# Performance work log

Hardware: AMD Instinct MI355X
Metric: run time of the kernel (lower is better)

## Reference

```python
import jax, jax.numpy as jnp
import numpy as np

B, T, D = 2, 2048, 2048
H, KVH = 16, 4
HD = D // H            # 128
HALF = HD // 2         # 64
EPS = 1e-6


def zc_rmsnorm(x, scale):
    # zero-centred RMSNorm: (1+scale) * x / rms(x), rms in fp32
    rms = jnp.sqrt(jnp.mean(x.astype(jnp.float32) ** 2, axis=-1, keepdims=True) + EPS)
    return ((1.0 + scale) * x / rms).astype(x.dtype)


def apply_rope(x, cos, sin):
    # x: [B, h, T, HD]; cos/sin: [T, HALF]
    t = x.shape[2]
    c = cos[:t][None, None, :, :]
    s = sin[:t][None, None, :, :]
    x1, x2 = x[..., :HALF], x[..., HALF:]
    return jnp.concatenate([x1 * c - x2 * s, x2 * c + x1 * s], axis=-1)


def setup_inputs() -> dict:
    key = jax.random.key(0)
    ks = jax.random.split(key, 8)
    std = 0.02
    res_std = 0.02 / np.sqrt(2 * 24)
    q_input = jax.random.normal(ks[0], (B, T, D), jnp.float32)
    kv_input = jax.random.normal(ks[1], (B, T, D), jnp.float32)
    mask = jnp.tril(jnp.ones((T, T), bool))[None, None, :, :]
    inv_freq = 1.0 / (10000.0 ** (jnp.arange(0, HALF, dtype=jnp.float32) / HALF))
    ang = jnp.arange(T, dtype=jnp.float32)[:, None] * inv_freq[None, :]
    cos, sin = jnp.cos(ang), jnp.sin(ang)
    Wq = jax.random.normal(ks[2], (D, D), jnp.float32) * std
    Wk = jax.random.normal(ks[3], (D, KVH * HD), jnp.float32) * std
    Wv = jax.random.normal(ks[4], (D, KVH * HD), jnp.float32) * std
    q_scale = jnp.zeros((HD,), jnp.float32)
    k_scale = jnp.zeros((HD,), jnp.float32)
    Wo = jax.random.normal(ks[5], (D, D), jnp.float32) * res_std
    return {"q_input": q_input, "kv_input": kv_input, "mask": mask,
            "cos": cos, "sin": sin, "Wq": Wq, "Wk": Wk, "Wv": Wv,
            "q_scale": q_scale, "k_scale": k_scale, "Wo": Wo}


def reference(q_input, kv_input, mask, cos, sin, Wq, Wk, Wv, q_scale, k_scale, Wo):
    b = q_input.shape[0]
    q = (q_input @ Wq).reshape(b, -1, H, HD).transpose(0, 2, 1, 3)      # [B,H,T,HD]
    k = (kv_input @ Wk).reshape(b, -1, KVH, HD).transpose(0, 2, 1, 3)   # [B,KVH,T,HD]
    v = (kv_input @ Wv).reshape(b, -1, KVH, HD).transpose(0, 2, 1, 3)
    q = zc_rmsnorm(q, q_scale)
    k = zc_rmsnorm(k, k_scale)
    rep = H // KVH
    k = jnp.repeat(k, rep, axis=1)
    v = jnp.repeat(v, rep, axis=1)
    q = apply_rope(q, cos, sin)
    k = apply_rope(k, cos, sin)
    scale = jnp.sqrt(jnp.float32(HD))
    scores = jnp.einsum('bhqd,bhkd->bhqk', q, k) / scale                # [B,H,T,T]
    scores = jnp.where(mask, scores, jnp.finfo(scores.dtype).min)
    attn = jax.nn.softmax(scores, axis=-1)
    out = jnp.einsum('bhqk,bhkd->bhqd', attn, v)
    out = out.transpose(0, 2, 1, 3).reshape(b, -1, D)
    return out @ Wo
```

## Files before the change

### kernel.cpp

```cpp
#include <hip/hip_runtime.h>

#define NB 2
#define NT 2048
#define ND 2048
#define NH 16
#define NKVH 4
#define NHD 128
#define NHALF 64
#define NREP (NH / NKVH)
#define MFIX 12.0f

typedef __bf16 bf16x8 __attribute__((ext_vector_type(8)));
typedef unsigned short u16x8 __attribute__((ext_vector_type(8)));
typedef float f32x4 __attribute__((ext_vector_type(4)));

__device__ __forceinline__ unsigned short f2b(float f) {
  union { float f; unsigned int u; } v; v.f = f;
  unsigned int r = v.u + 0x7FFFu + ((v.u >> 16) & 1u);
  return (unsigned short)(r >> 16);
}
__device__ __forceinline__ float b2f(unsigned short h) {
  union { unsigned int u; float f; } v; v.u = ((unsigned int)h) << 16;
  return v.f;
}

__device__ __forceinline__ void glds16(const unsigned short* g, unsigned short* l) {
  __builtin_amdgcn_global_load_lds(
      (__attribute__((address_space(1))) unsigned int*)(unsigned long long)g,
      (__attribute__((address_space(3))) unsigned int*)(unsigned int)(unsigned long long)l,
      16, 0, 0);
}

__device__ __forceinline__ void f2bf_body(const float* __restrict__ in,
                                          unsigned short* __restrict__ out, int lb) {
  const size_t i = (size_t)(lb * 256 + threadIdx.x) * 8;
  float4 a = *(const float4*)(in + i);
  float4 b = *(const float4*)(in + i + 4);
  u16x8 r;
  r[0] = f2b(a.x); r[1] = f2b(a.y); r[2] = f2b(a.z); r[3] = f2b(a.w);
  r[4] = f2b(b.x); r[5] = f2b(b.y); r[6] = f2b(b.z); r[7] = f2b(b.w);
  *(u16x8*)(out + i) = r;
}

__device__ __forceinline__ void wtrans_body(const float* __restrict__ in,
                                            unsigned short* __restrict__ out,
                                            int K, int N, int bx, int by,
                                            float (*tile)[33]) {
  const int k0 = by * 32, n0 = bx * 32;
  const int x = threadIdx.x & 31, y8 = threadIdx.x >> 5;
#pragma unroll
  for (int j = 0; j < 4; ++j) {
    const int y = y8 + j * 8;
    tile[y][x] = in[(size_t)(k0 + y) * N + n0 + x];
  }
  __syncthreads();
#pragma unroll
  for (int j = 0; j < 4; ++j) {
    const int y = y8 + j * 8;
    out[(size_t)(n0 + y) * K + k0 + x] = f2b(tile[x][y]);
  }
}

__global__ __launch_bounds__(256) void prep_all(const float* __restrict__ q_input,
                                                unsigned short* __restrict__ Qb16,
                                                const float* __restrict__ kv_input,
                                                unsigned short* __restrict__ KVb16,
                                                const float* __restrict__ Wq,
                                                unsigned short* __restrict__ Wqt,
                                                const float* __restrict__ Wk,
                                                const float* __restrict__ Wv,
                                                unsigned short* __restrict__ WkvT,
                                                const float* __restrict__ Wo,
                                                unsigned short* __restrict__ Wot) {
  __shared__ float tile[32][33];
  const int l = blockIdx.x;
  if (l < 4096) {
    f2bf_body(q_input, Qb16, l);
  } else if (l < 8192) {
    f2bf_body(kv_input, KVb16, l - 4096);
  } else if (l < 12288) {
    const int l2 = l - 8192;
    wtrans_body(Wq, Wqt, 2048, 2048, l2 & 63, l2 >> 6, tile);
  } else if (l < 13312) {
    const int l2 = l - 12288;
    wtrans_body(Wk, WkvT, 2048, 512, l2 & 15, l2 >> 4, tile);
  } else if (l < 14336) {
    const int l2 = l - 13312;
    wtrans_body(Wv, WkvT + (size_t)512 * 2048, 2048, 512, l2 & 15, l2 >> 4, tile);
  } else {
    const int l2 = l - 14336;
    wtrans_body(Wo, Wot, 2048, 2048, l2 & 63, l2 >> 6, tile);
  }
}

__device__ __forceinline__ void gemm_core(const unsigned short* __restrict__ A,
                                          const unsigned short* __restrict__ Bt,
                                          float* __restrict__ C,
                                          int N, int K, int m0, int n0,
                                          unsigned short* As, unsigned short* Bs) {
  const int tid = threadIdx.x;
  const int wave = tid >> 6, lane = tid & 63;
  const int wm = wave >> 1, wn = wave & 1;
  const int quad = lane >> 4, c = lane & 15;
  const int lr = lane >> 3;
  const int gsw = ((lane & 7) ^ lr) * 8;

  const unsigned short* pa[4];
  const unsigned short* pb[4];
  unsigned short* da[4];
  unsigned short* db[4];
#pragma unroll
  for (int j = 0; j < 4; ++j) {
    const int rb = j * 32 + wave * 8;
    pa[j] = A + (size_t)(m0 + rb + lr) * K + gsw;
    pb[j] = Bt + (size_t)(n0 + rb + lr) * K + gsw;
    da[j] = As + rb * 64;
    db[j] = Bs + rb * 64;
  }

  f32x4 acc[4][4] = {};
  const int nsteps = K >> 6;
  int cur = 0;

#pragma unroll
  for (int j = 0; j < 4; ++j) { glds16(pa[j], da[j]); glds16(pb[j], db[j]); }
  __syncthreads();

  for (int t = 0; t < nsteps; ++t) {
    const int nxt = (cur ^ 1) * (128 * 64);
    if (t + 1 < nsteps) {
      const int kn = (t + 1) << 6;
#pragma unroll
      for (int j = 0; j < 4; ++j) {
        glds16(pa[j] + kn, da[j] + nxt);
        glds16(pb[j] + kn, db[j] + nxt);
      }
    }
    const unsigned short* Ab = As + cur * (128 * 64);
    const unsigned short* Bb = Bs + cur * (128 * 64);
#pragma unroll
    for (int kk = 0; kk < 2; ++kk) {
      const int g = ((kk * 4 + quad) ^ (c & 7)) * 8;
      bf16x8 af[4];
#pragma unroll
      for (int sm = 0; sm < 4; ++sm)
        af[sm] = *(const bf16x8*)&Ab[(wm * 64 + sm * 16 + c) * 64 + g];
#pragma unroll
      for (int sn = 0; sn < 4; ++sn) {
        bf16x8 bfr = *(const bf16x8*)&Bb[(wn * 64 + sn * 16 + c) * 64 + g];
#pragma unroll
        for (int sm = 0; sm < 4; ++sm)
          acc[sm][sn] = __builtin_amdgcn_mfma_f32_16x16x32_bf16(af[sm], bfr, acc[sm][sn], 0, 0, 0);
      }
    }
    __syncthreads();
    cur ^= 1;
  }

#pragma unroll
  for (int sm = 0; sm < 4; ++sm)
#pragma unroll
    for (int sn = 0; sn < 4; ++sn) {
      const int row = m0 + wm * 64 + sm * 16 + quad * 4;
      const int col = n0 + wn * 64 + sn * 16 + c;
#pragma unroll
      for (int r = 0; r < 4; ++r)
        C[(size_t)(row + r) * N + col] = acc[sm][sn][r];
    }
}

__global__ __launch_bounds__(256) void gemm128(const unsigned short* __restrict__ A,
                                               const unsigned short* __restrict__ Bt,
                                               float* __restrict__ C,
                                               int M, int N, int K) {
  __shared__ unsigned short As[2 * 128 * 64];
  __shared__ unsigned short Bs[2 * 128 * 64];
  const int gx = gridDim.x;
  const int nwg = gx * gridDim.y;
  int lin = blockIdx.y * gx + blockIdx.x;
  lin = (lin & 7) * (nwg >> 3) + (lin >> 3);
  gemm_core(A, Bt, C, N, K, (lin / gx) * 128, (lin % gx) * 128, As, Bs);
}

__global__ __launch_bounds__(256) void gemm_qkv(const unsigned short* __restrict__ Aq,
                                                const unsigned short* __restrict__ Wq,
                                                float* __restrict__ Cq,
                                                const unsigned short* __restrict__ Akv,
                                                const unsigned short* __restrict__ Wkv,
                                                float* __restrict__ Ckv) {
  __shared__ unsigned short As[2 * 128 * 64];
  __shared__ unsigned short Bs[2 * 128 * 64];
  int lin = blockIdx.x;
  lin = (lin & 7) * 96 + (lin >> 3);
  if (lin < 512) {
    gemm_core(Aq, Wq, Cq, 2048, 2048, (lin >> 4) * 128, (lin & 15) * 128, As, Bs);
  } else {
    const int l2 = lin - 512;
    gemm_core(Akv, Wkv, Ckv, 1024, 2048, (l2 >> 3) * 128, (l2 & 7) * 128, As, Bs);
  }
}

__device__ __forceinline__ void rmsnorm_rope_body(const float* __restrict__ in,
                                                  unsigned short* __restrict__ out,
                                                  const float* __restrict__ scale,
                                                  const float* __restrict__ cosp,
                                                  const float* __restrict__ sinp,
                                                  int nh, int instride, float outscale,
                                                  int lb) {
  const int wid = lb * 4 + (threadIdx.x >> 6);
  const int lane = threadIdx.x & 63;
  const int h = wid % nh;
  const int t = (wid / nh) % NT;
  const int b = wid / (nh * NT);
  const float* x = in + (size_t)(b * NT + t) * instride + h * NHD;
  float x1 = x[lane], x2 = x[lane + NHALF];
  float ss = x1 * x1 + x2 * x2;
#pragma unroll
  for (int m = 1; m < 64; m <<= 1) ss += __shfl_xor(ss, m, 64);
  const float inv = 1.0f / sqrtf(ss * (1.0f / NHD) + 1e-6f);
  const float n1 = (1.0f + scale[lane]) * x1 * inv;
  const float n2 = (1.0f + scale[lane + NHALF]) * x2 * inv;
  const float cc = cosp[t * NHALF + lane], s = sinp[t * NHALF + lane];
  const size_t ob = (((size_t)b * nh + h) * NT + t) * NHD;
  out[ob + lane] = f2b((n1 * cc - n2 * s) * outscale);
  out[ob + lane + NHALF] = f2b((n2 * cc + n1 * s) * outscale);
}

__global__ __launch_bounds__(256) void fixup_all(const float* __restrict__ Q32,
                                                 unsigned short* __restrict__ Qh,
                                                 const float* __restrict__ KVp,
                                                 unsigned short* __restrict__ Kh,
                                                 unsigned short* __restrict__ Vtg,
                                                 const float* __restrict__ q_scale,
                                                 const float* __restrict__ k_scale,
                                                 const float* __restrict__ cosp,
                                                 const float* __restrict__ sinp) {
  __shared__ float tile[32][33];
  const int l = blockIdx.x;
  if (l < 16384) {
    rmsnorm_rope_body(Q32, Qh, q_scale, cosp, sinp, NH, ND, 0.08838834764831845f, l);
  } else if (l < 20480) {
    rmsnorm_rope_body(KVp, Kh, k_scale, cosp, sinp, NKVH, 1024, 1.0f, l - 16384);
  } else {
    const int l2 = l - 20480;
    const int bx = l2 & 63, by = (l2 >> 6) & 3, bg = l2 >> 8;
    const int b = bg >> 2, g = bg & 3;
    const int t0 = bx * 32, d0 = by * 32;
    const int x = threadIdx.x & 31, y8 = threadIdx.x >> 5;
    const float* vin = KVp + 512;
#pragma unroll
    for (int j = 0; j < 4; ++j) {
      const int y = y8 + j * 8;
      tile[y][x] = vin[(size_t)(b * NT + t0 + y) * 1024 + g * NHD + d0 + x];
    }
    __syncthreads();
#pragma unroll
    for (int j = 0; j < 4; ++j) {
      const int y = y8 + j * 8;
      Vtg[((size_t)bg * NHD + d0 + y) * NT + t0 + x] = f2b(tile[x][y]);
    }
  }
}

__global__ __launch_bounds__(256, 3) void attn64(const unsigned short* __restrict__ Qh,
                                                 const unsigned short* __restrict__ Kh,
                                                 const unsigned short* __restrict__ Vtg,
                                                 unsigned short* __restrict__ O) {
  __shared__ unsigned short Kt[64 * 132];
  __shared__ unsigned short Vt[128 * 68];
  __shared__ unsigned short Pt[64 * 68];
  const int bh = blockIdx.x;
  const int b = bh / NH, h = bh % NH, g = h / NREP;
  const int y = blockIdx.y;
  const int a = y & 7, bb = y >> 3;
  const int qt = (bb == 0) ? a : (bb == 1) ? a + 8 : (bb == 2) ? 31 - a : 23 - a;
  const int tid = threadIdx.x;
  const int w = tid >> 6, lane = tid & 63;
  const int quad = lane >> 4, c = lane & 15;

  bf16x8 qf[4];
  {
    const unsigned short* qp =
        Qh + ((size_t)(b * NH + h) * NT + qt * 64 + w * 16 + c) * NHD + quad * 8;
#pragma unroll
    for (int ch = 0; ch < 4; ++ch) qf[ch] = *(const bf16x8*)(qp + ch * 32);
  }

  f32x4 acc_o[8] = {};
  float lsum[4] = {0.f, 0.f, 0.f, 0.f};
  const size_t kbase = (size_t)(b * NKVH + g) * NT * NHD;
  const size_t vbase = (size_t)(b * NKVH + g) * NHD * NT;
  const int nkt = qt + 1;

  u16x8 kreg[4], vreg[4];
#pragma unroll
  for (int j = 0; j < 4; ++j) {
    const int f = j * 256 + tid;
    kreg[j] = *(const u16x8*)&Kh[kbase + (size_t)(f >> 4) * NHD + (f & 15) * 8];
    vreg[j] = *(const u16x8*)&Vtg[vbase + (size_t)(f >> 3) * NT + (f & 7) * 8];
  }

  for (int kt = 0; kt < nkt; ++kt) {
#pragma unroll
    for (int j = 0; j < 4; ++j) {
      const int f = j * 256 + tid;
      *(u16x8*)&Kt[(f >> 4) * 132 + (f & 15) * 8] = kreg[j];
      *(u16x8*)&Vt[(f >> 3) * 68 + (f & 7) * 8] = vreg[j];
    }
    __syncthreads();

    if (kt + 1 < nkt) {
      const int k0 = (kt + 1) * 64;
#pragma unroll
      for (int j = 0; j < 4; ++j) {
        const int f = j * 256 + tid;
        kreg[j] = *(const u16x8*)&Kh[kbase + (size_t)(k0 + (f >> 4)) * NHD + (f & 15) * 8];
        vreg[j] = *(const u16x8*)&Vtg[vbase + (size_t)(f >> 3) * NT + k0 + (f & 7) * 8];
      }
    }

    f32x4 s[4] = {};
#pragma unroll
    for (int n = 0; n < 4; ++n)
#pragma unroll
      for (int ch = 0; ch < 4; ++ch) {
        bf16x8 kf = *(const bf16x8*)&Kt[(n * 16 + c) * 132 + ch * 32 + quad * 8];
        s[n] = __builtin_amdgcn_mfma_f32_16x16x32_bf16(qf[ch], kf, s[n], 0, 0, 0);
      }

    const bool dmask = (kt == qt);
#pragma unroll
    for (int r = 0; r < 4; ++r) {
      float v0 = s[0][r], v1 = s[1][r], v2 = s[2][r], v3 = s[3][r];
      const int lrow = w * 16 + quad * 4 + r;
      if (dmask) {
        if (c > lrow) v0 = -1e30f;
        if (16 + c > lrow) v1 = -1e30f;
        if (32 + c > lrow) v2 = -1e30f;
        if (48 + c > lrow) v3 = -1e30f;
      }
      const float p0 = __expf(v0 - MFIX), p1 = __expf(v1 - MFIX);
      const float p2 = __expf(v2 - MFIX), p3 = __expf(v3 - MFIX);
      lsum[r] += (p0 + p1) + (p2 + p3);
      Pt[lrow * 68 + c] = f2b(p0);
      Pt[lrow * 68 + 16 + c] = f2b(p1);
      Pt[lrow * 68 + 32 + c] = f2b(p2);
      Pt[lrow * 68 + 48 + c] = f2b(p3);
    }

#pragma unroll
    for (int kc2 = 0; kc2 < 2; ++kc2) {
      bf16x8 pf = *(const bf16x8*)&Pt[(w * 16 + c) * 68 + kc2 * 32 + quad * 8];
#pragma unroll
      for (int n2 = 0; n2 < 8; ++n2) {
        bf16x8 vf = *(const bf16x8*)&Vt[(n2 * 16 + c) * 68 + kc2 * 32 + quad * 8];
        acc_o[n2] = __builtin_amdgcn_mfma_f32_16x16x32_bf16(pf, vf, acc_o[n2], 0, 0, 0);
      }
    }
    __syncthreads();
  }

#pragma unroll
  for (int r = 0; r < 4; ++r) {
    float l = lsum[r];
    l += __shfl_xor(l, 1, 64);
    l += __shfl_xor(l, 2, 64);
    l += __shfl_xor(l, 4, 64);
    l += __shfl_xor(l, 8, 64);
    lsum[r] = l;
  }

#pragma unroll
  for (int r = 0; r < 4; ++r) {
    const float invl = 1.0f / lsum[r];
    const int qrow = qt * 64 + w * 16 + quad * 4 + r;
    unsigned short* op = O + ((size_t)(b * NT + qrow) * NH + h) * NHD + c;
#pragma unroll
    for (int n2 = 0; n2 < 8; ++n2) op[n2 * 16] = f2b(acc_o[n2][r] * invl);
  }
}

extern "C" void kernel_launch(void* const* d_in, const int* in_sizes, int n_in,
                              void* d_out, int out_size, void* d_ws, size_t ws_size,
                              hipStream_t stream) {
  (void)in_sizes; (void)n_in; (void)out_size; (void)ws_size;
  const float* q_input  = (const float*)d_in[0];
  const float* kv_input = (const float*)d_in[1];
  const float* cosp = (const float*)d_in[3];
  const float* sinp = (const float*)d_in[4];
  const float* Wq = (const float*)d_in[5];
  const float* Wk = (const float*)d_in[6];
  const float* Wv = (const float*)d_in[7];
  const float* q_scale = (const float*)d_in[8];
  const float* k_scale = (const float*)d_in[9];
  const float* Wo = (const float*)d_in[10];
  float* out = (float*)d_out;

  char* p = (char*)d_ws;
  float* Q32  = (float*)p; p += (size_t)NB * NT * ND * 4;
  float* KVp  = (float*)p; p += (size_t)NB * NT * 1024 * 4;
  unsigned short* Qb16  = (unsigned short*)p; p += (size_t)NB * NT * ND * 2;
  unsigned short* KVb16 = (unsigned short*)p; p += (size_t)NB * NT * ND * 2;
  unsigned short* Kh  = (unsigned short*)p; p += (size_t)NB * NKVH * NT * NHD * 2;
  unsigned short* Vtg = (unsigned short*)p; p += (size_t)NB * NKVH * NT * NHD * 2;
  unsigned short* Wqt  = (unsigned short*)p; p += (size_t)ND * ND * 2;
  unsigned short* WkvT = (unsigned short*)p; p += (size_t)1024 * ND * 2;
  unsigned short* Wot  = (unsigned short*)p; p += (size_t)ND * ND * 2;
  unsigned short* Ob = Qb16;
  unsigned short* Qh = KVb16;

  const dim3 blk(256);
  const int M = NB * NT;

  prep_all<<<dim3(18432), blk, 0, stream>>>(q_input, Qb16, kv_input, KVb16,
                                            Wq, Wqt, Wk, Wv, WkvT, Wo, Wot);

  gemm_qkv<<<dim3(768), blk, 0, stream>>>(Qb16, Wqt, Q32, KVb16, WkvT, KVp);

  fixup_all<<<dim3(22528), blk, 0, stream>>>(Q32, Qh, KVp, Kh, Vtg,
                                             q_scale, k_scale, cosp, sinp);

  attn64<<<dim3(NB * NH, 32), blk, 0, stream>>>(Qh, Kh, Vtg, Ob);

  gemm128<<<dim3(ND / 128, M / 128), blk, 0, stream>>>(Ob, Wot, out, M, ND, ND);
}
```

Baseline: 354.8 us.

## Fuse RMSNorm, RoPE and V transpose into the QKV GEMM epilogue

The QKV GEMM now applies zero-centred RMSNorm and RoPE to each 128-wide head tile in its epilogue. It exchanges the partner half through shared memory and writes bf16 Q/K directly, and it transposes V into bf16 through LDS. This removes the fp32 Q/KV intermediates and the separate fixup kernel launch along with its global-memory round trip. The attention kernel also gains s_setprio hints around its MFMA sections. The cost is a heavier epilogue with an extra LDS pass and barrier in the GEMM, and Qh now gets its own workspace buffer.

```diff
diff --git a/kernel.cpp b/kernel.cpp
--- a/kernel.cpp
+++ b/kernel.cpp
@@ -12,16 +12,13 @@
 
 typedef __bf16 bf16x8 __attribute__((ext_vector_type(8)));
 typedef unsigned short u16x8 __attribute__((ext_vector_type(8)));
+typedef unsigned short u16x4 __attribute__((ext_vector_type(4)));
 typedef float f32x4 __attribute__((ext_vector_type(4)));
 
 __device__ __forceinline__ unsigned short f2b(float f) {
   union { float f; unsigned int u; } v; v.f = f;
   unsigned int r = v.u + 0x7FFFu + ((v.u >> 16) & 1u);
   return (unsigned short)(r >> 16);
-}
-__device__ __forceinline__ float b2f(unsigned short h) {
-  union { unsigned int u; float f; } v; v.u = ((unsigned int)h) << 16;
-  return v.f;
 }
 
 __device__ __forceinline__ void glds16(const unsigned short* g, unsigned short* l) {
@@ -93,11 +90,11 @@
   }
 }
 
-__device__ __forceinline__ void gemm_core(const unsigned short* __restrict__ A,
-                                          const unsigned short* __restrict__ Bt,
-                                          float* __restrict__ C,
-                                          int N, int K, int m0, int n0,
-                                          unsigned short* As, unsigned short* Bs) {
+__device__ __forceinline__ void gemm_mm(const unsigned short* __restrict__ A,
+                                        const unsigned short* __restrict__ Bt,
+                                        int K, int m0, int n0,
+                                        unsigned short* As, unsigned short* Bs,
+                                        f32x4 (&acc)[4][4]) {
   const int tid = threadIdx.x;
   const int wave = tid >> 6, lane = tid & 63;
   const int wm = wave >> 1, wn = wave & 1;
@@ -118,7 +115,12 @@
     db[j] = Bs + rb * 64;
   }
 
-  f32x4 acc[4][4] = {};
+  const f32x4 zero = {0.f, 0.f, 0.f, 0.f};
+#pragma unroll
+  for (int sm = 0; sm < 4; ++sm)
+#pragma unroll
+    for (int sn = 0; sn < 4; ++sn) acc[sm][sn] = zero;
+
   const int nsteps = K >> 6;
   int cur = 0;
 
@@ -156,108 +158,158 @@
     __syncthreads();
     cur ^= 1;
   }
-
-#pragma unroll
-  for (int sm = 0; sm < 4; ++sm)
-#pragma unroll
-    for (int sn = 0; sn < 4; ++sn) {
-      const int row = m0 + wm * 64 + sm * 16 + quad * 4;
-      const int col = n0 + wn * 64 + sn * 16 + c;
-#pragma unroll
-      for (int r = 0; r < 4; ++r)
-        C[(size_t)(row + r) * N + col] = acc[sm][sn][r];
-    }
 }
 
 __global__ __launch_bounds__(256) void gemm128(const unsigned short* __restrict__ A,
                                                const unsigned short* __restrict__ Bt,
                                                float* __restrict__ C,
                                                int M, int N, int K) {
-  __shared__ unsigned short As[2 * 128 * 64];
-  __shared__ unsigned short Bs[2 * 128 * 64];
+  __shared__ __align__(16) unsigned char smem[65536];
+  unsigned short* As = (unsigned short*)smem;
+  unsigned short* Bs = (unsigned short*)(smem + 32768);
   const int gx = gridDim.x;
   const int nwg = gx * gridDim.y;
   int lin = blockIdx.y * gx + blockIdx.x;
   lin = (lin & 7) * (nwg >> 3) + (lin >> 3);
-  gemm_core(A, Bt, C, N, K, (lin / gx) * 128, (lin % gx) * 128, As, Bs);
+  const int m0 = (lin / gx) * 128, n0 = (lin % gx) * 128;
+  f32x4 acc[4][4];
+  gemm_mm(A, Bt, K, m0, n0, As, Bs, acc);
+  const int tid = threadIdx.x;
+  const int wave = tid >> 6, lane = tid & 63;
+  const int wm = wave >> 1, wn = wave & 1;
+  const int quad = lane >> 4, c = lane & 15;
+#pragma unroll
+  for (int sm = 0; sm < 4; ++sm)
+#pragma unroll
+    for (int sn = 0; sn < 4; ++sn) {
+      const int row = m0 + wm * 64 + sm * 16 + quad * 4;
+      const int col = n0 + wn * 64 + sn * 16 + c;
+#pragma unroll
+      for (int r = 0; r < 4; ++r)
+        C[(size_t)(row + r) * N + col] = acc[sm][sn][r];
+    }
+}
+
+__device__ __forceinline__ void epi_normrope(f32x4 (&acc)[4][4], float* xb,
+                                             unsigned short* __restrict__ dst,
+                                             const float* __restrict__ scale,
+                                             const float* __restrict__ cosp,
+                                             const float* __restrict__ sinp,
+                                             int t0, float outscale) {
+  const int tid = threadIdx.x;
+  const int wave = tid >> 6, lane = tid & 63;
+  const int wm = wave >> 1, wn = wave & 1;
+  const int quad = lane >> 4, c = lane & 15;
+#pragma unroll
+  for (int sm = 0; sm < 4; ++sm)
+#pragma unroll
+    for (int sn = 0; sn < 4; ++sn) {
+      const int row = wm * 64 + sm * 16 + quad * 4;
+      const int col = wn * 64 + sn * 16 + c;
+#pragma unroll
+      for (int r = 0; r < 4; ++r)
+        xb[(row + r) * 128 + col] = acc[sm][sn][r];
+    }
+  __syncthreads();
+#pragma unroll
+  for (int sm = 0; sm < 4; ++sm) {
+#pragma unroll
+    for (int r = 0; r < 4; ++r) {
+      const int row = wm * 64 + sm * 16 + quad * 4 + r;
+      float par[4];
+      float ps = 0.f;
+#pragma unroll
+      for (int sn = 0; sn < 4; ++sn) {
+        const float own = acc[sm][sn][r];
+        par[sn] = xb[row * 128 + ((wn ^ 1) * 64 + sn * 16 + c)];
+        ps += own * own + par[sn] * par[sn];
+      }
+      ps += __shfl_xor(ps, 1, 64);
+      ps += __shfl_xor(ps, 2, 64);
+      ps += __shfl_xor(ps, 4, 64);
+      ps += __shfl_xor(ps, 8, 64);
+      const float inv = 1.0f / sqrtf(ps * (1.0f / NHD) + 1e-6f);
+      const int t = t0 + row;
+#pragma unroll
+      for (int sn = 0; sn < 4; ++sn) {
+        const int d = wn * 64 + sn * 16 + c;
+        const int dd = sn * 16 + c;
+        const float n_own = (1.0f + scale[d]) * acc[sm][sn][r] * inv;
+        const float n_par = (1.0f + scale[d ^ 64]) * par[sn] * inv;
+        const float cc = cosp[t * NHALF + dd], ss = sinp[t * NHALF + dd];
+        const float o = (wn == 0) ? (n_own * cc - n_par * ss)
+                                  : (n_own * cc + n_par * ss);
+        dst[(size_t)row * NHD + d] = f2b(o * outscale);
+      }
+    }
+  }
+}
+
+__device__ __forceinline__ void epi_vtrans(f32x4 (&acc)[4][4],
+                                           unsigned short* vb,
+                                           unsigned short* __restrict__ dst) {
+  const int tid = threadIdx.x;
+  const int wave = tid >> 6, lane = tid & 63;
+  const int wm = wave >> 1, wn = wave & 1;
+  const int quad = lane >> 4, c = lane & 15;
+#pragma unroll
+  for (int sm = 0; sm < 4; ++sm)
+#pragma unroll
+    for (int sn = 0; sn < 4; ++sn) {
+      const int row = wm * 64 + sm * 16 + quad * 4;
+      const int col = wn * 64 + sn * 16 + c;
+      u16x4 pk;
+      pk[0] = f2b(acc[sm][sn][0]); pk[1] = f2b(acc[sm][sn][1]);
+      pk[2] = f2b(acc[sm][sn][2]); pk[3] = f2b(acc[sm][sn][3]);
+      *(u16x4*)&vb[col * 136 + row] = pk;
+    }
+  __syncthreads();
+#pragma unroll
+  for (int i = 0; i < 32; ++i) {
+    const int d = wave * 32 + i;
+    const unsigned int v = *(const unsigned int*)&vb[d * 136 + lane * 2];
+    *(unsigned int*)&dst[(size_t)d * NT + lane * 2] = v;
+  }
 }
 
 __global__ __launch_bounds__(256) void gemm_qkv(const unsigned short* __restrict__ Aq,
-                                                const unsigned short* __restrict__ Wq,
-                                                float* __restrict__ Cq,
+                                                const unsigned short* __restrict__ Wqt,
                                                 const unsigned short* __restrict__ Akv,
                                                 const unsigned short* __restrict__ Wkv,
-                                                float* __restrict__ Ckv) {
-  __shared__ unsigned short As[2 * 128 * 64];
-  __shared__ unsigned short Bs[2 * 128 * 64];
+                                                unsigned short* __restrict__ Qh,
+                                                unsigned short* __restrict__ Kh,
+                                                unsigned short* __restrict__ Vtg,
+                                                const float* __restrict__ q_scale,
+                                                const float* __restrict__ k_scale,
+                                                const float* __restrict__ cosp,
+                                                const float* __restrict__ sinp) {
+  __shared__ __align__(16) unsigned char smem[65536];
+  unsigned short* As = (unsigned short*)smem;
+  unsigned short* Bs = (unsigned short*)(smem + 32768);
   int lin = blockIdx.x;
   lin = (lin & 7) * 96 + (lin >> 3);
+  f32x4 acc[4][4];
   if (lin < 512) {
-    gemm_core(Aq, Wq, Cq, 2048, 2048, (lin >> 4) * 128, (lin & 15) * 128, As, Bs);
+    const int m0 = (lin >> 4) * 128, n0 = (lin & 15) * 128;
+    gemm_mm(Aq, Wqt, 2048, m0, n0, As, Bs, acc);
+    const int b = m0 >> 11, t0 = m0 & 2047, h = n0 >> 7;
+    epi_normrope(acc, (float*)smem,
+                 Qh + ((size_t)(b * NH + h) * NT + t0) * NHD,
+                 q_scale, cosp, sinp, t0, 0.08838834764831845f);
   } else {
     const int l2 = lin - 512;
-    gemm_core(Akv, Wkv, Ckv, 1024, 2048, (l2 >> 3) * 128, (l2 & 7) * 128, As, Bs);
-  }
-}
-
-__device__ __forceinline__ void rmsnorm_rope_body(const float* __restrict__ in,
-                                                  unsigned short* __restrict__ out,
-                                                  const float* __restrict__ scale,
-                                                  const float* __restrict__ cosp,
-                                                  const float* __restrict__ sinp,
-                                                  int nh, int instride, float outscale,
-                                                  int lb) {
-  const int wid = lb * 4 + (threadIdx.x >> 6);
-  const int lane = threadIdx.x & 63;
-  const int h = wid % nh;
-  const int t = (wid / nh) % NT;
-  const int b = wid / (nh * NT);
-  const float* x = in + (size_t)(b * NT + t) * instride + h * NHD;
-  float x1 = x[lane], x2 = x[lane + NHALF];
-  float ss = x1 * x1 + x2 * x2;
-#pragma unroll
-  for (int m = 1; m < 64; m <<= 1) ss += __shfl_xor(ss, m, 64);
-  const float inv = 1.0f / sqrtf(ss * (1.0f / NHD) + 1e-6f);
-  const float n1 = (1.0f + scale[lane]) * x1 * inv;
-  const float n2 = (1.0f + scale[lane + NHALF]) * x2 * inv;
-  const float cc = cosp[t * NHALF + lane], s = sinp[t * NHALF + lane];
-  const size_t ob = (((size_t)b * nh + h) * NT + t) * NHD;
-  out[ob + lane] = f2b((n1 * cc - n2 * s) * outscale);
-  out[ob + lane + NHALF] = f2b((n2 * cc + n1 * s) * outscale);
-}
-
-__global__ __launch_bounds__(256) void fixup_all(const float* __restrict__ Q32,
-                                                 unsigned short* __restrict__ Qh,
-                                                 const float* __restrict__ KVp,
-                                                 unsigned short* __restrict__ Kh,
-                                                 unsigned short* __restrict__ Vtg,
-                                                 const float* __restrict__ q_scale,
-                                                 const float* __restrict__ k_scale,
-                                                 const float* __restrict__ cosp,
-                                                 const float* __restrict__ sinp) {
-  __shared__ float tile[32][33];
-  const int l = blockIdx.x;
-  if (l < 16384) {
-    rmsnorm_rope_body(Q32, Qh, q_scale, cosp, sinp, NH, ND, 0.08838834764831845f, l);
-  } else if (l < 20480) {
-    rmsnorm_rope_body(KVp, Kh, k_scale, cosp, sinp, NKVH, 1024, 1.0f, l - 16384);
-  } else {
-    const int l2 = l - 20480;
-    const int bx = l2 & 63, by = (l2 >> 6) & 3, bg = l2 >> 8;
-    const int b = bg >> 2, g = bg & 3;
-    const int t0 = bx * 32, d0 = by * 32;
-    const int x = threadIdx.x & 31, y8 = threadIdx.x >> 5;
-    const float* vin = KVp + 512;
-#pragma unroll
-    for (int j = 0; j < 4; ++j) {
-      const int y = y8 + j * 8;
-      tile[y][x] = vin[(size_t)(b * NT + t0 + y) * 1024 + g * NHD + d0 + x];
-    }
-    __syncthreads();
-#pragma unroll
-    for (int j = 0; j < 4; ++j) {
-      const int y = y8 + j * 8;
-      Vtg[((size_t)bg * NHD + d0 + y) * NT + t0 + x] = f2b(tile[x][y]);
+    const int m0 = (l2 >> 3) * 128, n0 = (l2 & 7) * 128;
+    gemm_mm(Akv, Wkv, 2048, m0, n0, As, Bs, acc);
+    const int b = m0 >> 11, t0 = m0 & 2047;
+    if (n0 < 512) {
+      const int g = n0 >> 7;
+      epi_normrope(acc, (float*)smem,
+                   Kh + ((size_t)(b * NKVH + g) * NT + t0) * NHD,
+                   k_scale, cosp, sinp, t0, 1.0f);
+    } else {
+      const int g = (n0 - 512) >> 7;
+      epi_vtrans(acc, (unsigned short*)smem,
+                 Vtg + ((size_t)(b * NKVH + g) * NHD) * NT + t0);
     }
   }
 }
@@ -320,6 +372,7 @@
     }
 
     f32x4 s[4] = {};
+    __builtin_amdgcn_s_setprio(1);
 #pragma unroll
     for (int n = 0; n < 4; ++n)
 #pragma unroll
@@ -327,6 +380,7 @@
         bf16x8 kf = *(const bf16x8*)&Kt[(n * 16 + c) * 132 + ch * 32 + quad * 8];
         s[n] = __builtin_amdgcn_mfma_f32_16x16x32_bf16(qf[ch], kf, s[n], 0, 0, 0);
       }
+    __builtin_amdgcn_s_setprio(0);
 
     const bool dmask = (kt == qt);
 #pragma unroll
@@ -348,6 +402,7 @@
       Pt[lrow * 68 + 48 + c] = f2b(p3);
     }
 
+    __builtin_amdgcn_s_setprio(1);
 #pragma unroll
     for (int kc2 = 0; kc2 < 2; ++kc2) {
       bf16x8 pf = *(const bf16x8*)&Pt[(w * 16 + c) * 68 + kc2 * 32 + quad * 8];
@@ -357,6 +412,7 @@
         acc_o[n2] = __builtin_amdgcn_mfma_f32_16x16x32_bf16(pf, vf, acc_o[n2], 0, 0, 0);
       }
     }
+    __builtin_amdgcn_s_setprio(0);
     __syncthreads();
   }
 
@@ -397,17 +453,15 @@
   float* out = (float*)d_out;
 
   char* p = (char*)d_ws;
-  float* Q32  = (float*)p; p += (size_t)NB * NT * ND * 4;
-  float* KVp  = (float*)p; p += (size_t)NB * NT * 1024 * 4;
   unsigned short* Qb16  = (unsigned short*)p; p += (size_t)NB * NT * ND * 2;
   unsigned short* KVb16 = (unsigned short*)p; p += (size_t)NB * NT * ND * 2;
+  unsigned short* Qh  = (unsigned short*)p; p += (size_t)NB * NH * NT * NHD * 2;
   unsigned short* Kh  = (unsigned short*)p; p += (size_t)NB * NKVH * NT * NHD * 2;
   unsigned short* Vtg = (unsigned short*)p; p += (size_t)NB * NKVH * NT * NHD * 2;
   unsigned short* Wqt  = (unsigned short*)p; p += (size_t)ND * ND * 2;
   unsigned short* WkvT = (unsigned short*)p; p += (size_t)1024 * ND * 2;
   unsigned short* Wot  = (unsigned short*)p; p += (size_t)ND * ND * 2;
   unsigned short* Ob = Qb16;
-  unsigned short* Qh = KVb16;
 
   const dim3 blk(256);
   const int M = NB * NT;
@@ -415,10 +469,8 @@
   prep_all<<<dim3(18432), blk, 0, stream>>>(q_input, Qb16, kv_input, KVb16,
                                             Wq, Wqt, Wk, Wv, WkvT, Wo, Wot);
 
-  gemm_qkv<<<dim3(768), blk, 0, stream>>>(Qb16, Wqt, Q32, KVb16, WkvT, KVp);
-
-  fixup_all<<<dim3(22528), blk, 0, stream>>>(Q32, Qh, KVp, Kh, Vtg,
-                                             q_scale, k_scale, cosp, sinp);
+  gemm_qkv<<<dim3(768), blk, 0, stream>>>(Qb16, Wqt, KVb16, WkvT,
+                                          Qh, Kh, Vtg, q_scale, k_scale, cosp, sinp);
 
   attn64<<<dim3(NB * NH, 32), blk, 0, stream>>>(Qh, Kh, Vtg, Ob);
 
```

After: 358.4 us. No clear change (+1.0%).
